# Performance work log

Measured on AMD Instinct MI355X. Metric: run time of the kernel, lower is better.

Reference implementation:

```python
import jax, jax.numpy as jnp
import numpy as np

H = 1024
E = 8
TOP_K = 2


def setup_inputs() -> dict:
    key = jax.random.key(0)
    ks = jax.random.split(key, 6)
    B, S = 4, 2048
    hidden_states = jax.random.normal(ks[0], (B, S, H), dtype=jnp.float32)
    # router weight, init N(0, 0.02)
    router_w = jax.random.normal(ks[1], (E, H), dtype=jnp.float32) * 0.02
    # stacked expert FFN params (nn.Linear: y = x @ W.T + b)
    lim = 1.0 / np.sqrt(H)
    W1 = jax.random.uniform(ks[2], (E, H, H), minval=-lim, maxval=lim, dtype=jnp.float32)
    b1 = jax.random.uniform(ks[3], (E, H), minval=-lim, maxval=lim, dtype=jnp.float32)
    W2 = jax.random.uniform(ks[4], (E, H, H), minval=-lim, maxval=lim, dtype=jnp.float32)
    b2 = jax.random.uniform(ks[5], (E, H), minval=-lim, maxval=lim, dtype=jnp.float32)
    return {"hidden_states": hidden_states, "router_w": router_w,
            "W1": W1, "b1": b1, "W2": W2, "b2": b2}


def reference(hidden_states, router_w, W1, b1, W2, b2):
    B, S, _ = hidden_states.shape
    # ---- router ----
    logits = jnp.einsum('bsh,eh->bse', hidden_states, router_w)  # [B,S,E]
    router_probs = jax.nn.softmax(logits.astype(jnp.float32), axis=-1)
    top_vals, top_idx = jax.lax.top_k(router_probs, TOP_K)        # [B,S,K]
    top_vals = top_vals / jnp.sum(top_vals, axis=-1, keepdims=True)  # norm_topk_prob
    # per-token per-expert combine weight (sum of top-k weights matching expert)
    w = jnp.sum(jax.nn.one_hot(top_idx, E, dtype=top_vals.dtype) * top_vals[..., None], axis=-2)  # [B,S,E]
    # ---- dense all-expert FFN (faithful to reference: every expert on every token) ----
    h1 = jax.nn.relu(jnp.einsum('bsh,efh->bsef', hidden_states, W1) + b1)   # [B,S,E,F]
    expert_out = jnp.einsum('bsef,egf->bseg', h1, W2) + b2                  # [B,S,E,H]
    moe_out = jnp.einsum('bseh,bse->bsh', expert_out, w)
    return hidden_states + moe_out, router_probs
```

## Files before the change

### kernel.cpp

```cpp
#include <hip/hip_runtime.h>
#include <hip/hip_bf16.h>


#define HD   1024
#define NTOK 8192
#define NEXP 8
#define BM   128
#define BN   128
#define BK   64
#define ZROW 8192
#define MAXP 17408
#define EP_LDSW 136

typedef __attribute__((ext_vector_type(8))) short  vshort8;
typedef __attribute__((ext_vector_type(4))) short  vshort4;
typedef __attribute__((ext_vector_type(4))) float  vfloat4;

typedef __attribute__((address_space(1))) const unsigned gas_uint;
typedef __attribute__((address_space(3))) unsigned       las_uint;

__device__ __forceinline__ void gld16(const void* g, void* l) {
    __builtin_amdgcn_global_load_lds((gas_uint*)g, (las_uint*)l, 16, 0, 0);
}

__device__ __forceinline__ short bf16r(float f) {
    union { float f; unsigned u; } a; a.f = f;
    unsigned r = a.u + 0x7FFFu + ((a.u >> 16) & 1u);
    return (short)(r >> 16);
}

__global__ void init_kernel(int* counts, int* fill, int* pair_token, short* xb) {
    int i = blockIdx.x * 256 + threadIdx.x;
    if (i < NEXP) { counts[i] = 0; fill[i] = 0; }
    if (i < MAXP) pair_token[i] = ZROW;
    if (i < HD / 8) {
        vshort8 z = {0, 0, 0, 0, 0, 0, 0, 0};
        *(vshort8*)(xb + (size_t)ZROW * HD + i * 8) = z;
    }
}

__global__ __launch_bounds__(256) void router_kernel(
    const float* __restrict__ x, const float* __restrict__ rw,
    float* __restrict__ out, short* __restrict__ xb,
    float* __restrict__ probs_out, int2* __restrict__ tok_top,
    float2* __restrict__ tok_w, int* __restrict__ counts) {
    __shared__ float rws[NEXP * HD];
    __shared__ int hist[NEXP];
    int t = threadIdx.x;
    if (t < NEXP) hist[t] = 0;
    for (int j = 0; j < 8; ++j) {
        int idx = j * 1024 + t * 4;
        *(vfloat4*)(rws + idx) = *(const vfloat4*)(rw + idx);
    }
    __syncthreads();
    int wave = t >> 6, lane = t & 63;
    for (int it = 0; it < 8; ++it) {
        int token = blockIdx.x * 32 + it * 4 + wave;
        const float* xr = x + (size_t)token * HD;
        float part[NEXP];
#pragma unroll
        for (int e = 0; e < NEXP; ++e) part[e] = 0.f;
        for (int j = 0; j < 4; ++j) {
            int off = j * 256 + lane * 4;
            vfloat4 xv = *(const vfloat4*)(xr + off);
            *(vfloat4*)(out + (size_t)token * HD + off) = xv;
            vshort4 bq;
            bq.x = bf16r(xv.x); bq.y = bf16r(xv.y); bq.z = bf16r(xv.z); bq.w = bf16r(xv.w);
            *(vshort4*)(xb + (size_t)token * HD + off) = bq;
#pragma unroll
            for (int e = 0; e < NEXP; ++e) {
                vfloat4 wv = *(const vfloat4*)(rws + e * HD + off);
                part[e] += xv.x * wv.x + xv.y * wv.y + xv.z * wv.z + xv.w * wv.w;
            }
        }
#pragma unroll
        for (int e = 0; e < NEXP; ++e)
            for (int off = 32; off; off >>= 1)
                part[e] += __shfl_xor(part[e], off, 64);
        if (lane == 0) {
            float m = part[0];
#pragma unroll
            for (int e = 1; e < NEXP; ++e) m = fmaxf(m, part[e]);
            float p[NEXP], s = 0.f;
#pragma unroll
            for (int e = 0; e < NEXP; ++e) { p[e] = expf(part[e] - m); s += p[e]; }
            float inv = 1.f / s;
#pragma unroll
            for (int e = 0; e < NEXP; ++e) {
                p[e] *= inv;
                probs_out[(size_t)token * NEXP + e] = p[e];
            }
            int i0 = 0;
#pragma unroll
            for (int e = 1; e < NEXP; ++e) if (p[e] > p[i0]) i0 = e;
            int i1 = (i0 == 0) ? 1 : 0;
#pragma unroll
            for (int e = 0; e < NEXP; ++e) if (e != i0 && p[e] > p[i1]) i1 = e;
            float s2 = 1.f / (p[i0] + p[i1]);
            tok_top[token] = make_int2(i0, i1);
            tok_w[token]   = make_float2(p[i0] * s2, p[i1] * s2);
            atomicAdd(&hist[i0], 1);
            atomicAdd(&hist[i1], 1);
        }
    }
    __syncthreads();
    if (t < NEXP) atomicAdd(&counts[t], hist[t]);
}

__global__ __launch_bounds__(256) void scatter_kernel(
    const int2* __restrict__ tok_top, const float2* __restrict__ tok_w,
    const int* __restrict__ counts, int* fill,
    int* __restrict__ pair_token, float* __restrict__ pair_w) {
    __shared__ int lhist[NEXP];
    __shared__ int lbase[NEXP];
    int t = threadIdx.x;
    if (t < NEXP) lhist[t] = 0;
    __syncthreads();
    int offs[NEXP];
    {
        int acc = 0;
#pragma unroll
        for (int f = 0; f < NEXP; ++f) {
            offs[f] = acc;
            acc += (counts[f] + 127) & ~127;
        }
    }
    int token = blockIdx.x * 256 + t;
    int2 ti = tok_top[token];
    float2 tw = tok_w[token];
    int r0 = atomicAdd(&lhist[ti.x], 1);
    int r1 = atomicAdd(&lhist[ti.y], 1);
    __syncthreads();
    if (t < NEXP) lbase[t] = atomicAdd(&fill[t], lhist[t]);
    __syncthreads();
    int s0 = offs[ti.x] + lbase[ti.x] + r0;
    pair_token[s0] = token; pair_w[s0] = tw.x;
    int s1 = offs[ti.y] + lbase[ti.y] + r1;
    pair_token[s1] = token; pair_w[s1] = tw.y;
}

__global__ void convw_kernel(const float* __restrict__ W1, const float* __restrict__ W2,
                             short* __restrict__ D1, short* __restrict__ D2) {
    size_t t = (size_t)blockIdx.x * 256 + threadIdx.x;
    const size_t PER = (size_t)NEXP * HD * HD / 8;
    const float* src = W1; short* dst = D1;
    if (t >= PER) { t -= PER; src = W2; dst = D2; }
    size_t C = t >> 6;
    int l  = (int)(t & 63);
    int kc = (int)(C & 31);
    int ng = (int)((C >> 5) & 63);
    int ei = (int)(C >> 11);
    int n = ng * 16 + (l & 15);
    int k = kc * 32 + (l >> 4) * 8;
    const float* s = src + ((size_t)ei * HD + n) * HD + k;
    vfloat4 a = *(const vfloat4*)s;
    vfloat4 b = *(const vfloat4*)(s + 4);
    vshort8 o;
    o[0] = bf16r(a.x); o[1] = bf16r(a.y); o[2] = bf16r(a.z); o[3] = bf16r(a.w);
    o[4] = bf16r(b.x); o[5] = bf16r(b.y); o[6] = bf16r(b.z); o[7] = bf16r(b.w);
    *(vshort8*)(dst + t * 8) = o;
}

template <int MODE>
__global__ __launch_bounds__(512, 4) void moe_gemm(
    const short* __restrict__ A, const short* __restrict__ Bw,
    const float* __restrict__ bias, const int* __restrict__ pair_token,
    const float* __restrict__ pair_w, const int* __restrict__ counts,
    short* __restrict__ h1sw_out, float* __restrict__ out) {
    __shared__ short smem[(MODE == 0) ? (BM * EP_LDSW) : (2 * BM * BK)];

    const int row0 = blockIdx.x * BM;
    int e = 0;
    {
        int csum = 0;
#pragma unroll
        for (int f = 0; f < NEXP; ++f) {
            int p = (counts[f] + 127) & ~127;
            if (csum + p <= row0) e = f + 1;
            csum += p;
        }
        if (row0 >= csum) return;
    }

    const int t = threadIdx.x;
    const int wave = t >> 6, lane = t & 63;
    const int wm = wave >> 2, wn = wave & 3;
    const int quad = lane >> 4, l16 = lane & 15;
    const int colb = blockIdx.y * BN;

    const char* agp;
    if (MODE == 0) {
        int tok = pair_token[row0 + wave * 16 + l16];
        agp = (const char*)A + (size_t)tok * (HD * 2) + quad * 16;
    } else {
        agp = (const char*)A + (((size_t)(row0 >> 4) + wave) * 32) * 1024 + lane * 16;
    }
    const char* bgp = (const char*)Bw +
        (((size_t)e * 64 + (colb >> 4) + wave) * 32) * 1024 + lane * 16;

    vfloat4 acc[4][2];
#pragma unroll
    for (int i = 0; i < 4; ++i)
#pragma unroll
        for (int j = 0; j < 2; ++j)
            acc[i][j] = (vfloat4){0.f, 0.f, 0.f, 0.f};

    for (int k0 = 0; k0 < HD; k0 += BK) {
        __syncthreads();
        const int kc = k0 >> 5;
#pragma unroll
        for (int s = 0; s < 2; ++s) {
            const char* ga = (MODE == 0)
                ? (agp + (size_t)k0 * 2 + s * 64)
                : (agp + (size_t)(kc + s) * 1024);
            gld16(ga, smem + (wave * 2 + s) * 512);
            gld16(bgp + (size_t)(kc + s) * 1024, smem + 8192 + (wave * 2 + s) * 512);
        }
        __syncthreads();
#pragma unroll
        for (int s = 0; s < 2; ++s) {
            vshort8 af[4], bfr[2];
#pragma unroll
            for (int i = 0; i < 4; ++i)
                af[i] = *(const vshort8*)(smem + ((wm * 4 + i) * 2 + s) * 512 + lane * 8);
#pragma unroll
            for (int j = 0; j < 2; ++j)
                bfr[j] = *(const vshort8*)(smem + 8192 + ((wn * 2 + j) * 2 + s) * 512 + lane * 8);
#pragma unroll
            for (int i = 0; i < 4; ++i)
#pragma unroll
                for (int j = 0; j < 2; ++j)
                    acc[i][j] = __builtin_amdgcn_mfma_f32_16x16x32_bf16(af[i], bfr[j], acc[i][j], 0, 0, 0);
        }
    }

    if (MODE == 0) {
        __syncthreads();
#pragma unroll
        for (int j = 0; j < 2; ++j) {
            int col = wn * 32 + j * 16 + l16;
            float bv = bias[e * HD + colb + col];
#pragma unroll
            for (int i = 0; i < 4; ++i) {
                int rl = wm * 64 + i * 16 + quad * 4;
#pragma unroll
                for (int reg = 0; reg < 4; ++reg) {
                    float v = acc[i][j][reg] + bv;
                    v = v > 0.f ? v : 0.f;
                    smem[(rl + reg) * EP_LDSW + col] = bf16r(v);
                }
            }
        }
        __syncthreads();
        int lrow = wave * 16 + l16;
#pragma unroll
        for (int kk = 0; kk < 4; ++kk) {
            vshort8 v = *(const vshort8*)(smem + lrow * EP_LDSW + kk * 32 + quad * 8);
            size_t chunk = ((size_t)((row0 >> 4) + wave) * 32) + ((colb >> 5) + kk);
            *(vshort8*)(h1sw_out + chunk * 512 + lane * 8) = v;
        }
    } else {
        int tok[4][4]; float wv[4][4];
#pragma unroll
        for (int i = 0; i < 4; ++i)
#pragma unroll
            for (int reg = 0; reg < 4; ++reg) {
                int r = row0 + wm * 64 + i * 16 + quad * 4 + reg;
                tok[i][reg] = pair_token[r];
                wv[i][reg] = pair_w[r];
            }
#pragma unroll
        for (int j = 0; j < 2; ++j) {
            int col = colb + wn * 32 + j * 16 + l16;
            float bv = bias[e * HD + col];
#pragma unroll
            for (int i = 0; i < 4; ++i)
#pragma unroll
                for (int reg = 0; reg < 4; ++reg)
                    if (tok[i][reg] < ZROW)
                        atomicAdd(out + (size_t)tok[i][reg] * HD + col,
                                  wv[i][reg] * (acc[i][j][reg] + bv));
        }
    }
}

extern "C" void kernel_launch(void* const* d_in, const int* in_sizes, int n_in,
                              void* d_out, int out_size, void* d_ws, size_t ws_size,
                              hipStream_t stream) {
    const float* x  = (const float*)d_in[0];
    const float* rw = (const float*)d_in[1];
    const float* W1 = (const float*)d_in[2];
    const float* b1 = (const float*)d_in[3];
    const float* W2 = (const float*)d_in[4];
    const float* b2 = (const float*)d_in[5];
    float* out   = (float*)d_out;
    float* probs = out + (size_t)NTOK * HD;

    char* ws = (char*)d_ws;
    short* xb = (short*)ws;            ws += (size_t)(NTOK + 1) * HD * 2;
    short* h1 = (short*)ws;            ws += (size_t)MAXP * HD * 2;
    int*   pair_token = (int*)ws;      ws += MAXP * 4;
    float* pair_w     = (float*)ws;    ws += MAXP * 4;
    int*   counts = (int*)ws;          ws += 256;
    int*   fill   = (int*)ws;          ws += 256;
    int2*   tok_top = (int2*)ws;       ws += NTOK * 8;
    float2* tok_w   = (float2*)ws;     ws += NTOK * 8;
    short* w1sw = (short*)ws;          ws += (size_t)NEXP * HD * HD * 2;
    short* w2sw = (short*)ws;          ws += (size_t)NEXP * HD * HD * 2;
    (void)ws_size;

    init_kernel<<<MAXP / 256, 256, 0, stream>>>(counts, fill, pair_token, xb);
    router_kernel<<<NTOK / 32, 256, 0, stream>>>(x, rw, out, xb, probs,
                                                 tok_top, tok_w, counts);
    scatter_kernel<<<NTOK / 256, 256, 0, stream>>>(tok_top, tok_w, counts, fill,
                                                   pair_token, pair_w);
    int cg = (int)(2 * ((size_t)NEXP * HD * HD / 8) / 256);
    convw_kernel<<<cg, 256, 0, stream>>>(W1, W2, w1sw, w2sw);
    dim3 gg(MAXP / BM, HD / BN);
    moe_gemm<0><<<gg, 512, 0, stream>>>(xb, w1sw, b1, pair_token, pair_w, counts, h1, nullptr);
    moe_gemm<1><<<gg, 512, 0, stream>>>(h1, w2sw, b2, pair_token, pair_w, counts, nullptr, out);
}
```

Baseline: 325.2 us.

## Double-buffer LDS tiles to overlap global loads with MFMA compute

Replaces the single-buffered K loop (sync, load, sync, compute) with a two-stage ping-pong LDS buffer. The next K tile is prefetched via global_load_lds while the current one is consumed, using explicit vmcnt waits and raw s_barrier. This hides global-load latency behind the MFMAs. In exchange, shared memory grows to 64 KB per block, which can lower occupancy below the four blocks per CU that the launch bounds request.

```diff
diff --git a/kernel.cpp b/kernel.cpp
--- a/kernel.cpp
+++ b/kernel.cpp
@@ -167,7 +167,7 @@
     const float* __restrict__ bias, const int* __restrict__ pair_token,
     const float* __restrict__ pair_w, const int* __restrict__ counts,
     short* __restrict__ h1sw_out, float* __restrict__ out) {
-    __shared__ short smem[(MODE == 0) ? (BM * EP_LDSW) : (2 * BM * BK)];
+    __shared__ short smem[32768];
 
     const int row0 = blockIdx.x * BM;
     int e = 0;
@@ -205,34 +205,54 @@
         for (int j = 0; j < 2; ++j)
             acc[i][j] = (vfloat4){0.f, 0.f, 0.f, 0.f};
 
-    for (int k0 = 0; k0 < HD; k0 += BK) {
-        __syncthreads();
-        const int kc = k0 >> 5;
-#pragma unroll
-        for (int s = 0; s < 2; ++s) {
-            const char* ga = (MODE == 0)
-                ? (agp + (size_t)k0 * 2 + s * 64)
-                : (agp + (size_t)(kc + s) * 1024);
-            gld16(ga, smem + (wave * 2 + s) * 512);
-            gld16(bgp + (size_t)(kc + s) * 1024, smem + 8192 + (wave * 2 + s) * 512);
-        }
-        __syncthreads();
+#define STAGE(bsel, kk0)                                                      \
+    {                                                                         \
+        const int kc_ = (kk0) >> 5;                                           \
+        short* sa_ = smem + (bsel) * 8192;                                    \
+        short* sb_ = smem + 16384 + (bsel) * 8192;                            \
+        _Pragma("unroll")                                                     \
+        for (int s = 0; s < 2; ++s) {                                         \
+            const char* ga_ = (MODE == 0)                                     \
+                ? (agp + (size_t)(kk0) * 2 + s * 64)                          \
+                : (agp + (size_t)(kc_ + s) * 1024);                           \
+            gld16(ga_, sa_ + (wave * 2 + s) * 512);                           \
+            gld16(bgp + (size_t)(kc_ + s) * 1024, sb_ + (wave * 2 + s) * 512);\
+        }                                                                     \
+    }
+
+    STAGE(0, 0)
+    int cur = 0;
+    for (int kt = 0; kt < HD / BK; ++kt) {
+        if (kt < HD / BK - 1) {
+            STAGE(cur ^ 1, (kt + 1) * BK)
+            asm volatile("s_waitcnt vmcnt(4)" ::: "memory");
+        } else {
+            asm volatile("s_waitcnt vmcnt(0)" ::: "memory");
+        }
+        __builtin_amdgcn_s_barrier();
+        asm volatile("" ::: "memory");
+        const short* sa = smem + cur * 8192;
+        const short* sb = smem + 16384 + cur * 8192;
 #pragma unroll
         for (int s = 0; s < 2; ++s) {
             vshort8 af[4], bfr[2];
 #pragma unroll
             for (int i = 0; i < 4; ++i)
-                af[i] = *(const vshort8*)(smem + ((wm * 4 + i) * 2 + s) * 512 + lane * 8);
+                af[i] = *(const vshort8*)(sa + ((wm * 4 + i) * 2 + s) * 512 + lane * 8);
 #pragma unroll
             for (int j = 0; j < 2; ++j)
-                bfr[j] = *(const vshort8*)(smem + 8192 + ((wn * 2 + j) * 2 + s) * 512 + lane * 8);
+                bfr[j] = *(const vshort8*)(sb + ((wn * 2 + j) * 2 + s) * 512 + lane * 8);
 #pragma unroll
             for (int i = 0; i < 4; ++i)
 #pragma unroll
                 for (int j = 0; j < 2; ++j)
                     acc[i][j] = __builtin_amdgcn_mfma_f32_16x16x32_bf16(af[i], bfr[j], acc[i][j], 0, 0, 0);
         }
-    }
+        asm volatile("" ::: "memory");
+        __builtin_amdgcn_s_barrier();
+        cur ^= 1;
+    }
+#undef STAGE
 
     if (MODE == 0) {
         __syncthreads();
```

Result: faster. 311.5 us (-4.2%).
